# Kernel optimization log

Measured on AMD Instinct MI355X. Metric: run time of the kernel, lower is better.

Reference implementation:

```python
import jax, jax.numpy as jnp
import numpy as np

B, S, HID = 1, 4096, 2048
NH, NKV, D = 16, 4, 128
BLK, M, K_TOP = 64, 32, 8
THETA = 10000.0
NEG = jnp.float32(-1e9)


def setup_inputs() -> dict:
    key = jax.random.key(0)
    ks = jax.random.split(key, 6)
    s = 0.02
    return {
        "hidden_states": jax.random.normal(ks[0], (B, S, HID), jnp.float32),
        "position_ids": jnp.arange(S, dtype=jnp.int32)[None, :],
        "Wq": jax.random.normal(ks[1], (HID, NH * D), jnp.float32) * s,
        "Wk": jax.random.normal(ks[2], (HID, NKV * D), jnp.float32) * s,
        "Wv": jax.random.normal(ks[3], (HID, NKV * D), jnp.float32) * s,
        "Wo": jax.random.normal(ks[4], (NH * D, HID), jnp.float32) * s,
        # seeded random-sign (Hadamard-style) sketch projection, non-trainable buffer
        "H_sketch": jnp.sign(jax.random.normal(ks[5], (D, M), jnp.float32)) / jnp.sqrt(jnp.float32(M)),
    }


def _rot_half(x):
    x1, x2 = x[..., : D // 2], x[..., D // 2 :]
    return jnp.concatenate([-x2, x1], axis=-1)


def reference(hidden_states, position_ids, Wq, Wk, Wv, Wo, H_sketch):
    # QKV projections -> [B, heads, S, D]
    q = (hidden_states @ Wq).reshape(B, S, NH, D).transpose(0, 2, 1, 3)
    k = (hidden_states @ Wk).reshape(B, S, NKV, D).transpose(0, 2, 1, 3)
    v = (hidden_states @ Wv).reshape(B, S, NKV, D).transpose(0, 2, 1, 3)

    # RoPE
    inv_freq = 1.0 / (THETA ** (jnp.arange(0, D, 2, dtype=jnp.float32) / D))
    freqs = position_ids.astype(jnp.float32)[:, :, None] * inv_freq[None, None, :]
    emb = jnp.concatenate([freqs, freqs], axis=-1)  # [B, S, D]
    cos, sin = jnp.cos(emb)[:, None], jnp.sin(emb)[:, None]  # [B, 1, S, D]
    q = q * cos + _rot_half(q) * sin
    k = k * cos + _rot_half(k) * sin

    # GQA repeat kv heads
    rep = NH // NKV
    k = jnp.repeat(k, rep, axis=1)
    v = jnp.repeat(v, rep, axis=1)

    nblk = S // BLK
    # Hadamard-sketch projections, block-mean pooled -> [B, NH, nblk, M]
    Sq = jnp.einsum("bhsd,dm->bhsm", q, H_sketch).reshape(B, NH, nblk, BLK, M).mean(axis=3)
    Sk = jnp.einsum("bhsd,dm->bhsm", k, H_sketch).reshape(B, NH, nblk, BLK, M).mean(axis=3)

    # Block-level sketch scores, causal at block granularity, diagonal forced in
    bs = jnp.einsum("bhim,bhjm->bhij", Sq, Sk)
    blk_causal = jnp.tril(jnp.ones((nblk, nblk), dtype=bool))
    bs = jnp.where(blk_causal, bs, NEG)
    bs = jnp.where(jnp.eye(nblk, dtype=bool), jnp.float32(1e9), bs)
    _, idx = jax.lax.top_k(bs, K_TOP)  # [B, NH, nblk, K_TOP]

    # Gather selected K/V blocks -> [B, NH, nblk, K_TOP, BLK, D]
    K5 = k.reshape(B, NH, nblk, BLK, D)
    V5 = v.reshape(B, NH, nblk, BLK, D)
    gidx = idx[..., None, None]
    Kg = jnp.take_along_axis(K5[:, :, None], gidx, axis=3)
    Vg = jnp.take_along_axis(V5[:, :, None], gidx, axis=3)

    # Block-sparse scores [B, NH, nblk, BLK, K_TOP, BLK]
    Qb = q.reshape(B, NH, nblk, BLK, D)
    scores = jnp.einsum("bhnqd,bhnkcd->bhnqkc", Qb, Kg) / jnp.sqrt(jnp.float32(D))

    # Token-level causal mask over gathered keys
    qpos = jnp.arange(nblk)[:, None] * BLK + jnp.arange(BLK)[None, :]  # [nblk, BLK]
    kpos = idx[..., None] * BLK + jnp.arange(BLK)  # [B, NH, nblk, K_TOP, BLK]
    mask = kpos[:, :, :, None] <= qpos[None, None, :, :, None, None]
    scores = jnp.where(mask, scores, NEG)

    probs = jax.nn.softmax(scores.reshape(B, NH, nblk, BLK, K_TOP * BLK), axis=-1)
    probs = probs.reshape(scores.shape)

    out = jnp.einsum("bhnqkc,bhnkcd->bhnqd", probs, Vg)
    out = out.reshape(B, NH, S, D).transpose(0, 2, 1, 3).reshape(B, S, NH * D)
    return out @ Wo
```

## Files before the change

### kernel.cpp

```cpp
#include <hip/hip_runtime.h>
#include <hip/hip_bf16.h>

#define S_LEN 4096
#define HID 2048
#define NH 16
#define NKV 4
#define HD 128
#define MSK 32
#define KTOP 8
#define NBLK 64
#define NEGV -1000000000.0f
#define SENT -3.0e38f

typedef __hip_bfloat16 bf16;
typedef __attribute__((ext_vector_type(8))) short short8;
typedef __attribute__((ext_vector_type(4))) float f32x4;


__device__ __forceinline__ unsigned short f2b(float v) {
    __hip_bfloat16 h = __float2bfloat16(v);
    return *reinterpret_cast<unsigned short*>(&h);
}
__device__ __forceinline__ float b2f(unsigned short u) {
    return __bfloat162float(*reinterpret_cast<__hip_bfloat16*>(&u));
}
__device__ __forceinline__ void gl16(const void* g, void* l) {
    __builtin_amdgcn_global_load_lds(
        (const __attribute__((address_space(1))) void*)g,
        (__attribute__((address_space(3))) void*)l, 16, 0, 0);
}

__global__ __launch_bounds__(256) void splitW_tiles(
    const float* __restrict__ Wq, const float* __restrict__ Wk,
    const float* __restrict__ Wv,
    bf16* __restrict__ WtqH, bf16* __restrict__ WtqL,
    bf16* __restrict__ WtkH, bf16* __restrict__ WtkL,
    bf16* __restrict__ WtvH) {
    const int u = blockIdx.x, kt = blockIdx.y, k0 = kt * 32;
    const float* W; char* TH; char* TL; int Nd, n0; bool hasLo;
    if (u < 16)      { W = Wq; TH = (char*)WtqH + (size_t)u * 524288;        TL = (char*)WtqL + (size_t)u * 524288; Nd = 2048; n0 = u * 128; hasLo = true; }
    else if (u < 20) { W = Wk; TH = (char*)WtkH + (size_t)(u - 16) * 524288; TL = (char*)WtkL + (size_t)(u - 16) * 524288; Nd = 512; n0 = (u - 16) * 128; hasLo = true; }
    else             { W = Wv; TH = (char*)WtvH + (size_t)(u - 20) * 524288; TL = nullptr; Nd = 512; n0 = (u - 20) * 128; hasLo = false; }
    __shared__ float Lw[32][132];
    const int t = threadIdx.x;
#pragma unroll
    for (int i = 0; i < 4; i++) {
        const int task = t + i * 256;
        const int k = task >> 5, c4 = task & 31;
        *(float4*)&Lw[k][c4 * 4] = *(const float4*)&W[(size_t)(k0 + k) * Nd + n0 + c4 * 4];
    }
    __syncthreads();
#pragma unroll
    for (int i = 0; i < 2; i++) {
        const int task = t + i * 256;
        const int col = task >> 2, lq = task & 3;
        alignas(16) unsigned short hh[8], lo[8];
#pragma unroll
        for (int j = 0; j < 8; j++) {
            const float x = Lw[lq * 8 + j][col];
            hh[j] = f2b(x);
            lo[j] = f2b(x - b2f(hh[j]));
        }
        const size_t off = (size_t)kt * 8192 + (size_t)(((col * 4 + lq) ^ (col & 7))) * 16;
        *(uint4*)(TH + off) = *(const uint4*)hh;
        if (hasLo) *(uint4*)(TL + off) = *(const uint4*)lo;
    }
}

__global__ __launch_bounds__(256) void splitT_Wo(const float* __restrict__ Wo,
                                                 bf16* __restrict__ WtoH) {
    const int n0 = blockIdx.x * 64, k0 = blockIdx.y * 64;
    __shared__ float Ls[64][68];
    const int t = threadIdx.x;
    {
        const int kk = t >> 2, c0 = (t & 3) * 16;
#pragma unroll
        for (int i = 0; i < 4; i++)
            *(float4*)&Ls[kk][c0 + i * 4] =
                *(const float4*)&Wo[(size_t)(k0 + kk) * HID + n0 + c0 + i * 4];
    }
    __syncthreads();
    const int c = t >> 2, ks = (t & 3) * 16;
    alignas(16) unsigned short hh[16];
#pragma unroll
    for (int j = 0; j < 16; j++) hh[j] = f2b(Ls[ks + j][c]);
    unsigned short* TH = (unsigned short*)WtoH;
    const size_t db = (size_t)(n0 + c) * HID + k0 + ks;
    *(uint4*)&TH[db + 0] = *(const uint4*)&hh[0];
    *(uint4*)&TH[db + 8] = *(const uint4*)&hh[8];
}

__global__ __launch_bounds__(256) void splitA_tiles(const float* __restrict__ A,
                                                    bf16* __restrict__ AhiT,
                                                    bf16* __restrict__ AloT) {
    const int rb = blockIdx.x, kt = blockIdx.y;
    const int t = threadIdx.x;
    char* DH = (char*)AhiT + ((size_t)rb * 64 + kt) * 8192;
    char* DL = (char*)AloT + ((size_t)rb * 64 + kt) * 8192;
#pragma unroll
    for (int i = 0; i < 2; i++) {
        const int task = t + i * 256;
        const int row = task >> 2, lq = task & 3;
        const float* ap = &A[(size_t)(rb * 128 + row) * HID + kt * 32 + lq * 8];
        const float4 v0 = *(const float4*)ap;
        const float4 v1 = *(const float4*)(ap + 4);
        const float f[8] = {v0.x, v0.y, v0.z, v0.w, v1.x, v1.y, v1.z, v1.w};
        alignas(16) unsigned short hh[8], lo[8];
#pragma unroll
        for (int j = 0; j < 8; j++) {
            hh[j] = f2b(f[j]);
            lo[j] = f2b(f[j] - b2f(hh[j]));
        }
        const size_t off = (size_t)(((row * 4 + lq) ^ (row & 7))) * 16;
        *(uint4*)(DH + off) = *(const uint4*)hh;
        *(uint4*)(DL + off) = *(const uint4*)lo;
    }
}

__global__ __launch_bounds__(256, 3) void proj4(
    const float* __restrict__ A,
    const bf16* __restrict__ AhiT_, const bf16* __restrict__ AloT_,
    const bf16* __restrict__ WtqH_, const bf16* __restrict__ WtqL_,
    const bf16* __restrict__ WtkH_, const bf16* __restrict__ WtkL_,
    const bf16* __restrict__ WtvH_,
    const int* __restrict__ pos_ids, const float* __restrict__ H,
    bf16* __restrict__ qf, bf16* __restrict__ kf, bf16* __restrict__ vfT,
    float* __restrict__ Sq, float* __restrict__ Sk) {
    const int u = blockIdx.x;
    const bool isQ = (u < 16);
    const bool isV = (u >= 20);
    const bool np3 = !isV;
    const int h = isQ ? u : (isV ? (u - 20) : (u - 16));
    const char* WHb = (const char*)(isQ ? WtqH_ : (isV ? WtvH_ : WtkH_)) + (size_t)h * 524288;
    const char* WLb = (const char*)(isQ ? WtqL_ : WtkL_) + (size_t)h * 524288;
    const char* AHb = (const char*)AhiT_;
    const char* ALb = (const char*)AloT_;
    bf16* __restrict__ Xout = isQ ? qf : kf;
    float* __restrict__ Sout = isQ ? Sq : Sk;
    const int Nd = isQ ? (NH * HD) : (NKV * HD);

    const int rb = blockIdx.y;
    const int m0g = rb * 128;
    const int t = threadIdx.x;
    const int w = t >> 6, L = t & 63;
    const int lm = L & 15, lq = L >> 4;

    __shared__ __align__(16) char arena[34816];
    __shared__ float red[4][128];
    char* Wh_s = arena;
    char* Wl_s = arena + 8192;
    char* Ah_s = arena + 16384;
    char* Al_s = arena + 24576;

    f32x4 acc[2][8];
#pragma unroll
    for (int mt = 0; mt < 2; mt++)
#pragma unroll
        for (int nt = 0; nt < 8; nt++) acc[mt][nt] = (f32x4){0.f, 0.f, 0.f, 0.f};

    for (int kt = 0; kt < 64; kt++) {
        __syncthreads();
        const size_t tW = (size_t)kt * 8192;
#pragma unroll
        for (int i = 0; i < 2; i++) {
            const int so = (w * 2 + i) * 1024;
            gl16(WHb + tW + so + L * 16, Wh_s + so);
            if (np3) gl16(WLb + tW + so + L * 16, Wl_s + so);
        }
        if (AHb) {
            const size_t tA = ((size_t)rb * 64 + kt) * 8192;
#pragma unroll
            for (int i = 0; i < 2; i++) {
                const int so = (w * 2 + i) * 1024;
                gl16(AHb + tA + so + L * 16, Ah_s + so);
                if (np3) gl16(ALb + tA + so + L * 16, Al_s + so);
            }
        } else {
            const int k0 = kt * 32;
#pragma unroll
            for (int i = 0; i < 2; i++) {
                const int task = t + i * 256;
                const int row = task >> 2, q2 = task & 3;
                const float* ap = &A[(size_t)(m0g + row) * HID + k0 + q2 * 8];
                const float4 v0 = *(const float4*)ap;
                const float4 v1 = *(const float4*)(ap + 4);
                const float f[8] = {v0.x, v0.y, v0.z, v0.w, v1.x, v1.y, v1.z, v1.w};
                alignas(16) unsigned short hh[8], lo[8];
#pragma unroll
                for (int j = 0; j < 8; j++) {
                    hh[j] = f2b(f[j]);
                    if (np3) lo[j] = f2b(f[j] - b2f(hh[j]));
                }
                const int ch = ((row * 4 + q2) ^ (row & 7)) * 16;
                *(uint4*)(Ah_s + ch) = *(const uint4*)hh;
                if (np3) *(uint4*)(Al_s + ch) = *(const uint4*)lo;
            }
        }
        __syncthreads();
        const int xr = lm & 7;
        short8 ah[2], al[2];
#pragma unroll
        for (int mt = 0; mt < 2; mt++) {
            const int rowA = w * 32 + mt * 16 + lm;
            const int cA = (((rowA * 4 + lq) ^ xr)) * 16;
            ah[mt] = *(const short8*)(Ah_s + cA);
            if (np3) al[mt] = *(const short8*)(Al_s + cA);
        }
#pragma unroll
        for (int nt = 0; nt < 8; nt++) {
            const int rowW = nt * 16 + lm;
            const int cW = (((rowW * 4 + lq) ^ xr)) * 16;
            const short8 bh = *(const short8*)(Wh_s + cW);
#pragma unroll
            for (int mt = 0; mt < 2; mt++)
                acc[mt][nt] = __builtin_amdgcn_mfma_f32_16x16x32_bf16(ah[mt], bh, acc[mt][nt], 0, 0, 0);
            if (np3) {
                const short8 bl = *(const short8*)(Wl_s + cW);
#pragma unroll
                for (int mt = 0; mt < 2; mt++) {
                    acc[mt][nt] = __builtin_amdgcn_mfma_f32_16x16x32_bf16(ah[mt], bl, acc[mt][nt], 0, 0, 0);
                    acc[mt][nt] = __builtin_amdgcn_mfma_f32_16x16x32_bf16(al[mt], bh, acc[mt][nt], 0, 0, 0);
                }
            }
        }
    }

    if (isV) {
        __syncthreads();
        unsigned short(*Tv)[136] = (unsigned short(*)[136])arena;
#pragma unroll
        for (int mt = 0; mt < 2; mt++) {
            const int rbs = w * 32 + mt * 16 + lq * 4;
#pragma unroll
            for (int rr = 0; rr < 4; rr++)
#pragma unroll
                for (int nt = 0; nt < 8; nt++)
                    Tv[nt * 16 + lm][rbs + rr] = f2b(acc[mt][nt][rr]);
        }
        __syncthreads();
        const int col = t >> 1, rh = (t & 1) * 64;
        bf16* dst = &vfT[((size_t)h * HD + col) * S_LEN + m0g + rh];
#pragma unroll
        for (int u2 = 0; u2 < 8; u2++)
            *(uint4*)&dst[u2 * 8] = *(const uint4*)&Tv[col][rh + u2 * 8];
        return;
    }

    {
        float invf[4];
#pragma unroll
        for (int c4 = 0; c4 < 4; c4++) {
            const int jj = c4 * 16 + lm;
            invf[c4] = 1.0f / powf(10000.0f, (float)jj * (1.0f / 64.0f));
        }
#pragma unroll
        for (int mt = 0; mt < 2; mt++) {
            const int rbase = w * 32 + mt * 16 + lq * 4;
#pragma unroll
            for (int rr = 0; rr < 4; rr++) {
                const float p = (float)pos_ids[m0g + rbase + rr];
#pragma unroll
                for (int c4 = 0; c4 < 4; c4++) {
                    const float fr = p * invf[c4];
                    float sv, cv;
                    sincosf(fr, &sv, &cv);
                    const float x1 = acc[mt][c4][rr];
                    const float x2 = acc[mt][c4 + 4][rr];
                    acc[mt][c4][rr]     = x1 * cv - x2 * sv;
                    acc[mt][c4 + 4][rr] = x2 * cv + x1 * sv;
                }
            }
        }
    }

    float cs[8];
#pragma unroll
    for (int nt = 0; nt < 8; nt++) cs[nt] = 0.f;
#pragma unroll
    for (int mt = 0; mt < 2; mt++) {
        const int rbase = w * 32 + mt * 16 + lq * 4;
#pragma unroll
        for (int rr = 0; rr < 4; rr++) {
            bf16* dst = &Xout[(size_t)(m0g + rbase + rr) * Nd + h * HD + lm];
#pragma unroll
            for (int nt = 0; nt < 8; nt++) {
                const float v = acc[mt][nt][rr];
                dst[nt * 16] = __float2bfloat16(v);
                cs[nt] += v;
            }
        }
    }
#pragma unroll
    for (int nt = 0; nt < 8; nt++) {
        cs[nt] += __shfl_xor(cs[nt], 16);
        cs[nt] += __shfl_xor(cs[nt], 32);
    }
    if (lq == 0) {
#pragma unroll
        for (int nt = 0; nt < 8; nt++) red[w][nt * 16 + lm] = cs[nt];
    }
    __syncthreads();
    if (t < 64) {
        const int b = t >> 5, m = t & 31;
        float s = 0.f;
        for (int d = 0; d < 128; d++)
            s += (red[b * 2][d] + red[b * 2 + 1][d]) * H[d * MSK + m];
        Sout[((size_t)h * NBLK + (m0g >> 6) + b) * MSK + m] = s * (1.0f / 64.0f);
    }
}

__global__ __launch_bounds__(256, 3) void proj_rope_sketch(
    const float* __restrict__ A, const float* __restrict__ Wq,
    const float* __restrict__ Wk, const float* __restrict__ Wv,
    const int* __restrict__ pos_ids, const float* __restrict__ H,
    bf16* __restrict__ qf, bf16* __restrict__ kf, bf16* __restrict__ vf,
    float* __restrict__ Sq, float* __restrict__ Sk,
    int u0, int r0, int xbase) {
    const int u = blockIdx.x + u0;
    const bool isQ = (u < 16);
    const bool isV = (u >= 20);
    const bool np3 = !isV;
    const int h = isQ ? u : (isV ? (u - 20) : (u - 16));
    const float* __restrict__ W = isQ ? Wq : (isV ? Wv : Wk);
    const int Nd = isQ ? (NH * HD) : (NKV * HD);
    bf16* __restrict__ Xout = isQ ? qf : kf;
    float* __restrict__ Sout = isQ ? Sq : Sk;

    const int m0g = r0 + blockIdx.y * 128;
    const int m0x = isQ ? (m0g - xbase) : m0g;
    const int t = threadIdx.x;
    const int w = t >> 6, L = t & 63;
    const int lm = L & 15, lq = L >> 4;

    __shared__ __align__(16) unsigned short shmem[4 * 128 * 40];
    __shared__ float red[4][128];
    unsigned short(*pAh)[40] = (unsigned short(*)[40])(shmem);
    unsigned short(*pAl)[40] = (unsigned short(*)[40])(shmem + 128 * 40);
    unsigned short(*pWh)[40] = (unsigned short(*)[40])(shmem + 2 * 128 * 40);
    unsigned short(*pWl)[40] = (unsigned short(*)[40])(shmem + 3 * 128 * 40);

    f32x4 acc[2][8];
#pragma unroll
    for (int mt = 0; mt < 2; mt++)
#pragma unroll
        for (int nt = 0; nt < 8; nt++) acc[mt][nt] = (f32x4){0.f, 0.f, 0.f, 0.f};

    for (int k0 = 0; k0 < HID; k0 += 32) {
        __syncthreads();
#pragma unroll
        for (int i = 0; i < 4; i++) {
            const int idx = t + i * 256;
            const int row = idx >> 3, f4 = idx & 7;
            const float4 v = *(const float4*)&A[(size_t)(m0g + row) * HID + k0 + f4 * 4];
            ushort4 uh;
            uh.x = f2b(v.x); uh.y = f2b(v.y); uh.z = f2b(v.z); uh.w = f2b(v.w);
            *(ushort4*)&pAh[row][f4 * 4] = uh;
            if (np3) {
                ushort4 ul;
                ul.x = f2b(v.x - b2f(uh.x)); ul.y = f2b(v.y - b2f(uh.y));
                ul.z = f2b(v.z - b2f(uh.z)); ul.w = f2b(v.w - b2f(uh.w));
                *(ushort4*)&pAl[row][f4 * 4] = ul;
            }
        }
        {
            const int wcol = t >> 1, wk0 = (t & 1) * 16;
            const float* wp = &W[(size_t)(k0 + wk0) * Nd + h * HD + wcol];
            alignas(16) unsigned short hh[16];
            alignas(16) unsigned short ll[16];
#pragma unroll
            for (int uu = 0; uu < 16; uu++) {
                const float x = wp[(size_t)uu * Nd];
                hh[uu] = f2b(x);
                ll[uu] = f2b(x - b2f(hh[uu]));
            }
            *(uint4*)&pWh[wcol][wk0 + 0] = *(const uint4*)&hh[0];
            *(uint4*)&pWh[wcol][wk0 + 8] = *(const uint4*)&hh[8];
            if (np3) {
                *(uint4*)&pWl[wcol][wk0 + 0] = *(const uint4*)&ll[0];
                *(uint4*)&pWl[wcol][wk0 + 8] = *(const uint4*)&ll[8];
            }
        }
        __syncthreads();
        short8 ah[2], al[2];
#pragma unroll
        for (int mt = 0; mt < 2; mt++) {
            ah[mt] = *(const short8*)&pAh[w * 32 + mt * 16 + lm][lq * 8];
            if (np3) al[mt] = *(const short8*)&pAl[w * 32 + mt * 16 + lm][lq * 8];
        }
#pragma unroll
        for (int nt = 0; nt < 8; nt++) {
            const short8 bh = *(const short8*)&pWh[nt * 16 + lm][lq * 8];
#pragma unroll
            for (int mt = 0; mt < 2; mt++)
                acc[mt][nt] = __builtin_amdgcn_mfma_f32_16x16x32_bf16(ah[mt], bh, acc[mt][nt], 0, 0, 0);
            if (np3) {
                const short8 bl = *(const short8*)&pWl[nt * 16 + lm][lq * 8];
#pragma unroll
                for (int mt = 0; mt < 2; mt++) {
                    acc[mt][nt] = __builtin_amdgcn_mfma_f32_16x16x32_bf16(ah[mt], bl, acc[mt][nt], 0, 0, 0);
                    acc[mt][nt] = __builtin_amdgcn_mfma_f32_16x16x32_bf16(al[mt], bh, acc[mt][nt], 0, 0, 0);
                }
            }
        }
    }

    if (isV) {
        __syncthreads();
        unsigned short(*Tv)[136] = (unsigned short(*)[136])shmem;
#pragma unroll
        for (int mt = 0; mt < 2; mt++) {
            const int rbs = w * 32 + mt * 16 + lq * 4;
#pragma unroll
            for (int rr = 0; rr < 4; rr++)
#pragma unroll
                for (int nt = 0; nt < 8; nt++)
                    Tv[nt * 16 + lm][rbs + rr] = f2b(acc[mt][nt][rr]);
        }
        __syncthreads();
        const int col = t >> 1, rh = (t & 1) * 64;
        bf16* dst = &vf[((size_t)h * HD + col) * S_LEN + m0g + rh];
#pragma unroll
        for (int u2 = 0; u2 < 8; u2++)
            *(uint4*)&dst[u2 * 8] = *(const uint4*)&Tv[col][rh + u2 * 8];
        return;
    }

    {
        float invf[4];
#pragma unroll
        for (int c4 = 0; c4 < 4; c4++) {
            const int jj = c4 * 16 + lm;
            invf[c4] = 1.0f / powf(10000.0f, (float)jj * (1.0f / 64.0f));
        }
#pragma unroll
        for (int mt = 0; mt < 2; mt++) {
            const int rbase = w * 32 + mt * 16 + lq * 4;
#pragma unroll
            for (int rr = 0; rr < 4; rr++) {
                const float p = (float)pos_ids[m0g + rbase + rr];
#pragma unroll
                for (int c4 = 0; c4 < 4; c4++) {
                    const float fr = p * invf[c4];
                    float sv, cv;
                    sincosf(fr, &sv, &cv);
                    const float x1 = acc[mt][c4][rr];
                    const float x2 = acc[mt][c4 + 4][rr];
                    acc[mt][c4][rr]     = x1 * cv - x2 * sv;
                    acc[mt][c4 + 4][rr] = x2 * cv + x1 * sv;
                }
            }
        }
    }

    float cs[8];
#pragma unroll
    for (int nt = 0; nt < 8; nt++) cs[nt] = 0.f;
#pragma unroll
    for (int mt = 0; mt < 2; mt++) {
        const int rbase = w * 32 + mt * 16 + lq * 4;
#pragma unroll
        for (int rr = 0; rr < 4; rr++) {
            bf16* dst = &Xout[(size_t)(m0x + rbase + rr) * Nd + h * HD + lm];
#pragma unroll
            for (int nt = 0; nt < 8; nt++) {
                const float v = acc[mt][nt][rr];
                dst[nt * 16] = __float2bfloat16(v);
                cs[nt] += v;
            }
        }
    }
#pragma unroll
    for (int nt = 0; nt < 8; nt++) {
        cs[nt] += __shfl_xor(cs[nt], 16);
        cs[nt] += __shfl_xor(cs[nt], 32);
    }
    if (lq == 0) {
#pragma unroll
        for (int nt = 0; nt < 8; nt++) red[w][nt * 16 + lm] = cs[nt];
    }
    __syncthreads();
    if (t < 64) {
        const int b = t >> 5, m = t & 31;
        float s = 0.f;
        for (int d = 0; d < 128; d++)
            s += (red[b * 2][d] + red[b * 2 + 1][d]) * H[d * MSK + m];
        Sout[((size_t)h * NBLK + (m0g >> 6) + b) * MSK + m] = s * (1.0f / 64.0f);
    }
}

__global__ __launch_bounds__(64) void topk_kernel(const float* __restrict__ Sq,
                                                  const float* __restrict__ Sk,
                                                  int* __restrict__ topk, int i0) {
    const int i = i0 + blockIdx.x, h = blockIdx.y, kv = h >> 2;
    const int j = threadIdx.x;
    __shared__ float vals[64];
    float v;
    if (j > i) v = NEGV;
    else if (j == i) v = 1e9f;
    else {
        v = 0.f;
        const float* sq = Sq + ((size_t)h * NBLK + i) * MSK;
        const float* sk = Sk + ((size_t)kv * NBLK + j) * MSK;
        for (int m = 0; m < MSK; m++) v += sq[m] * sk[m];
    }
    vals[j] = v;
    __syncthreads();
    if (j == 0) {
        for (int kk = 0; kk < KTOP; kk++) {
            float best = SENT; int bi = 0;
            for (int jj = 0; jj < 64; jj++)
                if (vals[jj] > best) { best = vals[jj]; bi = jj; }
            vals[bi] = SENT;
            topk[((size_t)h * NBLK + i) * KTOP + kk] = bi;
        }
    }
}

__global__ __launch_bounds__(256) void attn_kernel(bf16* __restrict__ qf,
                                                   const bf16* __restrict__ kf,
                                                   const bf16* __restrict__ vfT,
                                                   const int* __restrict__ topk,
                                                   int r0, int qbase) {
    const int qbg = (r0 >> 6) + blockIdx.x;
    const int h = blockIdx.y, kvh = h >> 2;
    const int t = threadIdx.x;
    const int w = t >> 6, L = t & 63;
    const int lm = L & 15, lq = L >> 4;

    __shared__ __align__(16) unsigned short Ks[64][136];
    __shared__ __align__(16) unsigned short Vt[128][72];
    __shared__ __align__(16) unsigned short Ps[64][72];

    short8 qfrag[4];
    {
        const size_t qrow = (size_t)(qbg * 64 - qbase) + w * 16 + lm;
        const unsigned short* qp = (const unsigned short*)qf + qrow * (NH * HD) + h * HD;
#pragma unroll
        for (int ks = 0; ks < 4; ks++)
            qfrag[ks] = *(const short8*)&qp[ks * 32 + lq * 8];
    }
    f32x4 O[8];
#pragma unroll
    for (int nt = 0; nt < 8; nt++) O[nt] = (f32x4){0.f, 0.f, 0.f, 0.f};
    f32x4 mrow = (f32x4){-1e30f, -1e30f, -1e30f, -1e30f};
    f32x4 lrow = (f32x4){0.f, 0.f, 0.f, 0.f};

    const int* sel = topk + ((size_t)h * NBLK + qbg) * KTOP;
    const int qpos0 = qbg * 64 + w * 16 + lq * 4;
    const float scale = 0.08838834764831845f;

    for (int kb = 0; kb < KTOP; kb++) {
        const int blk = sel[kb] & 63;
        __syncthreads();
#pragma unroll
        for (int i = 0; i < 4; i++) {
            const int idx = t + i * 256;
            const int rr = idx >> 4, c8 = idx & 15;
            *(uint4*)&Ks[rr][c8 * 8] =
                *(const uint4*)&kf[(size_t)(blk * 64 + rr) * (NKV * HD) + kvh * HD + c8 * 8];
        }
#pragma unroll
        for (int i = 0; i < 4; i++) {
            const int idx = t + i * 256;
            const int dd = idx >> 3, j8 = idx & 7;
            *(uint4*)&Vt[dd][j8 * 8] =
                *(const uint4*)&vfT[((size_t)kvh * HD + dd) * S_LEN + blk * 64 + j8 * 8];
        }
        __syncthreads();
        f32x4 S4[4];
#pragma unroll
        for (int nt = 0; nt < 4; nt++) {
            S4[nt] = (f32x4){0.f, 0.f, 0.f, 0.f};
#pragma unroll
            for (int ks = 0; ks < 4; ks++) {
                const short8 bk = *(const short8*)&Ks[nt * 16 + lm][ks * 32 + lq * 8];
                S4[nt] = __builtin_amdgcn_mfma_f32_16x16x32_bf16(qfrag[ks], bk, S4[nt], 0, 0, 0);
            }
        }
#pragma unroll
        for (int nt = 0; nt < 4; nt++) {
            const int kpos = blk * 64 + nt * 16 + lm;
#pragma unroll
            for (int r = 0; r < 4; r++)
                S4[nt][r] = (kpos <= qpos0 + r) ? S4[nt][r] * scale : NEGV;
        }
        f32x4 mx = S4[0];
#pragma unroll
        for (int nt = 1; nt < 4; nt++)
#pragma unroll
            for (int r = 0; r < 4; r++) mx[r] = fmaxf(mx[r], S4[nt][r]);
#pragma unroll
        for (int d = 1; d < 16; d <<= 1)
#pragma unroll
            for (int r = 0; r < 4; r++) mx[r] = fmaxf(mx[r], __shfl_xor(mx[r], d));
        f32x4 mnew, alv, sum;
#pragma unroll
        for (int r = 0; r < 4; r++) {
            mnew[r] = fmaxf(mrow[r], mx[r]);
            alv[r] = __expf(mrow[r] - mnew[r]);
            sum[r] = 0.f;
        }
#pragma unroll
        for (int nt = 0; nt < 4; nt++)
#pragma unroll
            for (int r = 0; r < 4; r++) {
                const float p = __expf(S4[nt][r] - mnew[r]);
                S4[nt][r] = p;
                sum[r] += p;
            }
#pragma unroll
        for (int d = 1; d < 16; d <<= 1)
#pragma unroll
            for (int r = 0; r < 4; r++) sum[r] += __shfl_xor(sum[r], d);
#pragma unroll
        for (int r = 0; r < 4; r++) {
            lrow[r] = lrow[r] * alv[r] + sum[r];
            mrow[r] = mnew[r];
        }
#pragma unroll
        for (int nt = 0; nt < 4; nt++)
#pragma unroll
            for (int r = 0; r < 4; r++)
                Ps[w * 16 + lq * 4 + r][nt * 16 + lm] = f2b(S4[nt][r]);
#pragma unroll
        for (int nt = 0; nt < 8; nt++)
#pragma unroll
            for (int r = 0; r < 4; r++) O[nt][r] *= alv[r];
#pragma unroll
        for (int ks2 = 0; ks2 < 2; ks2++) {
            const short8 pa = *(const short8*)&Ps[w * 16 + lm][ks2 * 32 + lq * 8];
#pragma unroll
            for (int nt = 0; nt < 8; nt++) {
                const short8 vv = *(const short8*)&Vt[nt * 16 + lm][ks2 * 32 + lq * 8];
                O[nt] = __builtin_amdgcn_mfma_f32_16x16x32_bf16(pa, vv, O[nt], 0, 0, 0);
            }
        }
    }
    f32x4 inv;
#pragma unroll
    for (int r = 0; r < 4; r++) inv[r] = 1.0f / lrow[r];
    const size_t orow0 = (size_t)(qbg * 64 - qbase) + w * 16 + lq * 4;
#pragma unroll
    for (int nt = 0; nt < 8; nt++)
#pragma unroll
        for (int r = 0; r < 4; r++)
            qf[(orow0 + r) * (NH * HD) + h * HD + nt * 16 + lm] =
                __float2bfloat16(O[nt][r] * inv[r]);
}

__global__ __launch_bounds__(256) void gemm_out(const bf16* __restrict__ A,
                                                const float* __restrict__ W,
                                                float* __restrict__ C, int cRow0) {
    __shared__ __align__(16) unsigned short Wl[128][40];
    const int n0 = blockIdx.x * 128, m0 = blockIdx.y * 128;
    const int t = threadIdx.x;
    const int w = t >> 6, L = t & 63;
    const int lm = L & 15, lq = L >> 4;
    const int wcol = t >> 1, wk0 = (t & 1) * 16;
    f32x4 acc[2][8];
#pragma unroll
    for (int mt = 0; mt < 2; mt++)
#pragma unroll
        for (int nt = 0; nt < 8; nt++) acc[mt][nt] = (f32x4){0.f, 0.f, 0.f, 0.f};

    float wreg[16];
    {
        const float* wp = &W[(size_t)wk0 * HID + n0 + wcol];
#pragma unroll
        for (int u = 0; u < 16; u++) wreg[u] = wp[(size_t)u * HID];
    }
    short8 av[2];
#pragma unroll
    for (int mt = 0; mt < 2; mt++)
        av[mt] = *(const short8*)&A[(size_t)(m0 + w * 32 + mt * 16 + lm) * HID + lq * 8];

    for (int k0 = 0; k0 < HID; k0 += 32) {
        __syncthreads();
        {
            alignas(16) unsigned short hh[16];
#pragma unroll
            for (int u = 0; u < 16; u++) hh[u] = f2b(wreg[u]);
            *(uint4*)&Wl[wcol][wk0 + 0] = *(const uint4*)&hh[0];
            *(uint4*)&Wl[wcol][wk0 + 8] = *(const uint4*)&hh[8];
        }
        const int k1 = k0 + 32;
        if (k1 < HID) {
            const float* wp = &W[(size_t)(k1 + wk0) * HID + n0 + wcol];
#pragma unroll
            for (int u = 0; u < 16; u++) wreg[u] = wp[(size_t)u * HID];
        }
        __syncthreads();
        short8 avn[2];
        if (k1 < HID) {
#pragma unroll
            for (int mt = 0; mt < 2; mt++)
                avn[mt] = *(const short8*)&A[(size_t)(m0 + w * 32 + mt * 16 + lm) * HID + k1 + lq * 8];
        }
#pragma unroll
        for (int nt = 0; nt < 8; nt++) {
            const short8 bv = *(const short8*)&Wl[nt * 16 + lm][lq * 8];
#pragma unroll
            for (int mt = 0; mt < 2; mt++)
                acc[mt][nt] = __builtin_amdgcn_mfma_f32_16x16x32_bf16(av[mt], bv, acc[mt][nt], 0, 0, 0);
        }
        if (k1 < HID) { av[0] = avn[0]; av[1] = avn[1]; }
    }
#pragma unroll
    for (int mt = 0; mt < 2; mt++)
#pragma unroll
        for (int nt = 0; nt < 8; nt++)
#pragma unroll
            for (int r = 0; r < 4; r++) {
                const int row = m0 + w * 32 + mt * 16 + lq * 4 + r;
                C[(size_t)(cRow0 + row) * HID + n0 + nt * 16 + lm] = acc[mt][nt][r];
            }
}

__global__ __launch_bounds__(256) void gemm_out2(const bf16* __restrict__ A,
                                                 const bf16* __restrict__ WtoH,
                                                 float* __restrict__ C) {
    __shared__ __align__(16) unsigned short Wl[128][72];
    const int n0 = blockIdx.x * 128, m0 = blockIdx.y * 128;
    const int t = threadIdx.x;
    const int w = t >> 6, L = t & 63;
    const int lm = L & 15, lq = L >> 4;
    const int ct = t >> 1, sg = (t & 1) * 32;
    const unsigned short* __restrict__ WT = (const unsigned short*)WtoH;
    f32x4 acc[2][8];
#pragma unroll
    for (int mt = 0; mt < 2; mt++)
#pragma unroll
        for (int nt = 0; nt < 8; nt++) acc[mt][nt] = (f32x4){0.f, 0.f, 0.f, 0.f};

    uint4 wbuf[4];
    {
        const unsigned short* wp = &WT[(size_t)(n0 + ct) * HID + sg];
#pragma unroll
        for (int i = 0; i < 4; i++) wbuf[i] = *(const uint4*)&wp[i * 8];
    }
    short8 av[2][2];
#pragma unroll
    for (int mt = 0; mt < 2; mt++)
#pragma unroll
        for (int ks = 0; ks < 2; ks++)
            av[mt][ks] = *(const short8*)&A[(size_t)(m0 + w * 32 + mt * 16 + lm) * HID + ks * 32 + lq * 8];

    for (int k0 = 0; k0 < HID; k0 += 64) {
        __syncthreads();
#pragma unroll
        for (int i = 0; i < 4; i++) *(uint4*)&Wl[ct][sg + i * 8] = wbuf[i];
        const int k1 = k0 + 64;
        if (k1 < HID) {
            const unsigned short* wp = &WT[(size_t)(n0 + ct) * HID + k1 + sg];
#pragma unroll
            for (int i = 0; i < 4; i++) wbuf[i] = *(const uint4*)&wp[i * 8];
        }
        __syncthreads();
        short8 avn[2][2];
        if (k1 < HID) {
#pragma unroll
            for (int mt = 0; mt < 2; mt++)
#pragma unroll
                for (int ks = 0; ks < 2; ks++)
                    avn[mt][ks] = *(const short8*)&A[(size_t)(m0 + w * 32 + mt * 16 + lm) * HID + k1 + ks * 32 + lq * 8];
        }
#pragma unroll
        for (int ks = 0; ks < 2; ks++)
#pragma unroll
            for (int nt = 0; nt < 8; nt++) {
                const short8 bv = *(const short8*)&Wl[nt * 16 + lm][ks * 32 + lq * 8];
#pragma unroll
                for (int mt = 0; mt < 2; mt++)
                    acc[mt][nt] = __builtin_amdgcn_mfma_f32_16x16x32_bf16(av[mt][ks], bv, acc[mt][nt], 0, 0, 0);
            }
        if (k1 < HID) {
#pragma unroll
            for (int mt = 0; mt < 2; mt++)
#pragma unroll
                for (int ks = 0; ks < 2; ks++) av[mt][ks] = avn[mt][ks];
        }
    }
#pragma unroll
    for (int mt = 0; mt < 2; mt++)
#pragma unroll
        for (int nt = 0; nt < 8; nt++)
#pragma unroll
            for (int r = 0; r < 4; r++) {
                const int row = m0 + w * 32 + mt * 16 + lq * 4 + r;
                C[(size_t)row * HID + n0 + nt * 16 + lm] = acc[mt][nt][r];
            }
}

extern "C" void kernel_launch(void* const* d_in, const int* in_sizes, int n_in,
                              void* d_out, int out_size, void* d_ws, size_t ws_size,
                              hipStream_t stream) {
    const void *p_hid, *p_pos, *p_wq, *p_wk, *p_wv, *p_wo, *p_h;
    if (in_sizes[0] == 4096 && in_sizes[1] == 1048576) {
        p_h = d_in[0]; p_wk = d_in[1]; p_wo = d_in[2]; p_wq = d_in[3];
        p_wv = d_in[4]; p_hid = d_in[5]; p_pos = d_in[6];
    } else {
        p_hid = d_in[0]; p_pos = d_in[1]; p_wq = d_in[2]; p_wk = d_in[3];
        p_wv = d_in[4]; p_wo = d_in[5]; p_h = d_in[6];
    }
    const float* hidden = (const float*)p_hid;
    const int* pos_ids  = (const int*)p_pos;
    const float* Wq = (const float*)p_wq;
    const float* Wk = (const float*)p_wk;
    const float* Wv = (const float*)p_wv;
    const float* Wo = (const float*)p_wo;
    const float* Hsk = (const float*)p_h;
    float* out = (float*)d_out;

    char* base = (char*)d_ws;
    float* Sq    = (float*)base;
    float* Sk    = (float*)(base + 131072);
    int*   topkb = (int*)(base + 163840);
    bf16*  kf    = (bf16*)(base + 196608);
    bf16*  vfT   = (bf16*)(base + 196608 + 4194304);
    bf16*  qbuf  = (bf16*)(base + 196608 + 8388608);
    bf16*  WtqH  = (bf16*)(base + 25362432);
    bf16*  WtqL  = (bf16*)(base + 33751040);
    bf16*  WtkH  = (bf16*)(base + 42139648);
    bf16*  WtkL  = (bf16*)(base + 44236800);
    bf16*  WtvH  = (bf16*)(base + 46333952);
    bf16*  WtoH  = (bf16*)(base + 48431104);
    bf16*  AhiT  = (bf16*)(base + 56819712);
    bf16*  AloT  = (bf16*)(base + 73596928);
    const size_t FULL_NEED  = 25362432;
    const size_t FULL2_NEED = 48431104;
    const size_t FULL3_NEED = 56819712;
    const size_t FULL4_NEED = 90374144;

    if (ws_size >= FULL2_NEED) {
        const bool hasWo = (ws_size >= FULL3_NEED);
        const bool hasA  = (ws_size >= FULL4_NEED);
        splitW_tiles<<<dim3(24, 64), 256, 0, stream>>>(
            Wq, Wk, Wv, WtqH, WtqL, WtkH, WtkL, WtvH);
        if (hasWo)
            splitT_Wo<<<dim3(32, 32), 256, 0, stream>>>(Wo, WtoH);
        if (hasA)
            splitA_tiles<<<dim3(32, 64), 256, 0, stream>>>(hidden, AhiT, AloT);
        proj4<<<dim3(24, 32), 256, 0, stream>>>(
            hidden, hasA ? AhiT : nullptr, hasA ? AloT : nullptr,
            WtqH, WtqL, WtkH, WtkL, WtvH, pos_ids, Hsk,
            qbuf, kf, vfT, Sq, Sk);
        topk_kernel<<<dim3(NBLK, NH), 64, 0, stream>>>(Sq, Sk, topkb, 0);
        attn_kernel<<<dim3(NBLK, NH), 256, 0, stream>>>(
            qbuf, kf, vfT, topkb, 0, 0);
        if (hasWo)
            gemm_out2<<<dim3(HID / 128, S_LEN / 128), 256, 0, stream>>>(
                qbuf, WtoH, out);
        else
            gemm_out<<<dim3(HID / 128, S_LEN / 128), 256, 0, stream>>>(
                qbuf, Wo, out, 0);
    } else if (ws_size >= FULL_NEED) {
        proj_rope_sketch<<<dim3(24, S_LEN / 128), 256, 0, stream>>>(
            hidden, Wq, Wk, Wv, pos_ids, Hsk, qbuf, kf, vfT, Sq, Sk, 0, 0, 0);
        topk_kernel<<<dim3(NBLK, NH), 64, 0, stream>>>(Sq, Sk, topkb, 0);
        attn_kernel<<<dim3(NBLK, NH), 256, 0, stream>>>(
            qbuf, kf, vfT, topkb, 0, 0);
        gemm_out<<<dim3(HID / 128, S_LEN / 128), 256, 0, stream>>>(
            qbuf, Wo, out, 0);
    } else {
        proj_rope_sketch<<<dim3(8, S_LEN / 128), 256, 0, stream>>>(
            hidden, Wq, Wk, Wv, pos_ids, Hsk, qbuf, kf, vfT, Sq, Sk, 16, 0, 0);
        for (int c = 0; c < 16; c++) {
            const int r0 = c * 256;
            proj_rope_sketch<<<dim3(16, 2), 256, 0, stream>>>(
                hidden, Wq, Wk, Wv, pos_ids, Hsk, qbuf, kf, vfT, Sq, Sk, 0, r0, r0);
            topk_kernel<<<dim3(4, NH), 64, 0, stream>>>(Sq, Sk, topkb, r0 >> 6);
            attn_kernel<<<dim3(4, NH), 256, 0, stream>>>(
                qbuf, kf, vfT, topkb, r0, r0);
            gemm_out<<<dim3(HID / 128, 2), 256, 0, stream>>>(
                qbuf, Wo, out, r0);
        }
    }
}
```

Measured before the change: 460.9 us.

## Swizzle block ids for XCD locality, prefetch K/V in attention, shrink output GEMM tile

The projection, attention and output GEMM kernels now use a 1-D grid, and each kernel remaps its block id with an XCD-style swizzle. The intent is for blocks that share weights or KV heads to run on the same chiplet and hit the same L2. The attention kernel register-prefetches the next selected K/V block while computing on the current one, and raises wave priority around the MFMA sections. The output GEMM tile narrows from 128 to 64 columns, doubling the block count to 1024 for better occupancy, at the cost of less reuse of A per block.

```diff
diff --git a/kernel.cpp b/kernel.cpp
--- a/kernel.cpp
+++ b/kernel.cpp
@@ -126,7 +126,10 @@
     const int* __restrict__ pos_ids, const float* __restrict__ H,
     bf16* __restrict__ qf, bf16* __restrict__ kf, bf16* __restrict__ vfT,
     float* __restrict__ Sq, float* __restrict__ Sk) {
-    const int u = blockIdx.x;
+    const int id = blockIdx.x;
+    const int swz = (id & 7) * 96 + (id >> 3);
+    const int u = swz >> 5;
+    const int rb = swz & 31;
     const bool isQ = (u < 16);
     const bool isV = (u >= 20);
     const bool np3 = !isV;
@@ -139,7 +142,6 @@
     float* __restrict__ Sout = isQ ? Sq : Sk;
     const int Nd = isQ ? (NH * HD) : (NKV * HD);
 
-    const int rb = blockIdx.y;
     const int m0g = rb * 128;
     const int t = threadIdx.x;
     const int w = t >> 6, L = t & 63;
@@ -521,8 +523,17 @@
                                                    const bf16* __restrict__ vfT,
                                                    const int* __restrict__ topk,
                                                    int r0, int qbase) {
-    const int qbg = (r0 >> 6) + blockIdx.x;
-    const int h = blockIdx.y, kvh = h >> 2;
+    int qbg, h;
+    if (gridDim.y == 1) {
+        const int id = blockIdx.x;
+        const int swz = (id & 7) * 128 + (id >> 3);
+        h = swz >> 6;
+        qbg = swz & 63;
+    } else {
+        qbg = (r0 >> 6) + blockIdx.x;
+        h = blockIdx.y;
+    }
+    const int kvh = h >> 2;
     const int t = threadIdx.x;
     const int w = t >> 6, L = t & 63;
     const int lm = L & 15, lq = L >> 4;
@@ -549,25 +560,38 @@
     const int qpos0 = qbg * 64 + w * 16 + lq * 4;
     const float scale = 0.08838834764831845f;
 
+    const int rrK0 = t >> 4, c8K = t & 15;
+    const int ddV0 = t >> 3, j8V = t & 7;
+    uint4 kreg[4], vreg[4];
+    int blk = sel[0] & 63;
+    {
+#pragma unroll
+        for (int i = 0; i < 4; i++)
+            kreg[i] = *(const uint4*)&kf[(size_t)(blk * 64 + rrK0 + i * 16) * (NKV * HD) + kvh * HD + c8K * 8];
+#pragma unroll
+        for (int i = 0; i < 4; i++)
+            vreg[i] = *(const uint4*)&vfT[((size_t)kvh * HD + ddV0 + i * 32) * S_LEN + blk * 64 + j8V * 8];
+    }
+
     for (int kb = 0; kb < KTOP; kb++) {
-        const int blk = sel[kb] & 63;
-        __syncthreads();
-#pragma unroll
-        for (int i = 0; i < 4; i++) {
-            const int idx = t + i * 256;
-            const int rr = idx >> 4, c8 = idx & 15;
-            *(uint4*)&Ks[rr][c8 * 8] =
-                *(const uint4*)&kf[(size_t)(blk * 64 + rr) * (NKV * HD) + kvh * HD + c8 * 8];
-        }
-#pragma unroll
-        for (int i = 0; i < 4; i++) {
-            const int idx = t + i * 256;
-            const int dd = idx >> 3, j8 = idx & 7;
-            *(uint4*)&Vt[dd][j8 * 8] =
-                *(const uint4*)&vfT[((size_t)kvh * HD + dd) * S_LEN + blk * 64 + j8 * 8];
-        }
-        __syncthreads();
+        const int cur_blk = blk;
+        __syncthreads();
+#pragma unroll
+        for (int i = 0; i < 4; i++) *(uint4*)&Ks[rrK0 + i * 16][c8K * 8] = kreg[i];
+#pragma unroll
+        for (int i = 0; i < 4; i++) *(uint4*)&Vt[ddV0 + i * 32][j8V * 8] = vreg[i];
+        __syncthreads();
+        if (kb + 1 < KTOP) {
+            blk = sel[kb + 1] & 63;
+#pragma unroll
+            for (int i = 0; i < 4; i++)
+                kreg[i] = *(const uint4*)&kf[(size_t)(blk * 64 + rrK0 + i * 16) * (NKV * HD) + kvh * HD + c8K * 8];
+#pragma unroll
+            for (int i = 0; i < 4; i++)
+                vreg[i] = *(const uint4*)&vfT[((size_t)kvh * HD + ddV0 + i * 32) * S_LEN + blk * 64 + j8V * 8];
+        }
         f32x4 S4[4];
+        __builtin_amdgcn_s_setprio(1);
 #pragma unroll
         for (int nt = 0; nt < 4; nt++) {
             S4[nt] = (f32x4){0.f, 0.f, 0.f, 0.f};
@@ -577,9 +601,10 @@
                 S4[nt] = __builtin_amdgcn_mfma_f32_16x16x32_bf16(qfrag[ks], bk, S4[nt], 0, 0, 0);
             }
         }
+        __builtin_amdgcn_s_setprio(0);
 #pragma unroll
         for (int nt = 0; nt < 4; nt++) {
-            const int kpos = blk * 64 + nt * 16 + lm;
+            const int kpos = cur_blk * 64 + nt * 16 + lm;
 #pragma unroll
             for (int r = 0; r < 4; r++)
                 S4[nt][r] = (kpos <= qpos0 + r) ? S4[nt][r] * scale : NEGV;
@@ -626,6 +651,7 @@
         for (int nt = 0; nt < 8; nt++)
 #pragma unroll
             for (int r = 0; r < 4; r++) O[nt][r] *= alv[r];
+        __builtin_amdgcn_s_setprio(1);
 #pragma unroll
         for (int ks2 = 0; ks2 < 2; ks2++) {
             const short8 pa = *(const short8*)&Ps[w * 16 + lm][ks2 * 32 + lq * 8];
@@ -635,6 +661,7 @@
                 O[nt] = __builtin_amdgcn_mfma_f32_16x16x32_bf16(pa, vv, O[nt], 0, 0, 0);
             }
         }
+        __builtin_amdgcn_s_setprio(0);
     }
     f32x4 inv;
 #pragma unroll
@@ -719,24 +746,27 @@
 __global__ __launch_bounds__(256) void gemm_out2(const bf16* __restrict__ A,
                                                  const bf16* __restrict__ WtoH,
                                                  float* __restrict__ C) {
-    __shared__ __align__(16) unsigned short Wl[128][72];
-    const int n0 = blockIdx.x * 128, m0 = blockIdx.y * 128;
+    const int id = blockIdx.x;
+    const int swz = (id & 7) * 128 + (id >> 3);
+    const int rb = swz >> 5, np = swz & 31;
+    const int n0 = np * 64, m0 = rb * 128;
+    __shared__ __align__(16) unsigned short Wl[64][72];
     const int t = threadIdx.x;
     const int w = t >> 6, L = t & 63;
     const int lm = L & 15, lq = L >> 4;
-    const int ct = t >> 1, sg = (t & 1) * 32;
+    const int ct = t >> 2, sg = (t & 3) * 16;
     const unsigned short* __restrict__ WT = (const unsigned short*)WtoH;
-    f32x4 acc[2][8];
+    f32x4 acc[2][4];
 #pragma unroll
     for (int mt = 0; mt < 2; mt++)
 #pragma unroll
-        for (int nt = 0; nt < 8; nt++) acc[mt][nt] = (f32x4){0.f, 0.f, 0.f, 0.f};
-
-    uint4 wbuf[4];
+        for (int nt = 0; nt < 4; nt++) acc[mt][nt] = (f32x4){0.f, 0.f, 0.f, 0.f};
+
+    uint4 wbuf[2];
     {
         const unsigned short* wp = &WT[(size_t)(n0 + ct) * HID + sg];
-#pragma unroll
-        for (int i = 0; i < 4; i++) wbuf[i] = *(const uint4*)&wp[i * 8];
+        wbuf[0] = *(const uint4*)&wp[0];
+        wbuf[1] = *(const uint4*)&wp[8];
     }
     short8 av[2][2];
 #pragma unroll
@@ -747,13 +777,13 @@
 
     for (int k0 = 0; k0 < HID; k0 += 64) {
         __syncthreads();
-#pragma unroll
-        for (int i = 0; i < 4; i++) *(uint4*)&Wl[ct][sg + i * 8] = wbuf[i];
+        *(uint4*)&Wl[ct][sg + 0] = wbuf[0];
+        *(uint4*)&Wl[ct][sg + 8] = wbuf[1];
         const int k1 = k0 + 64;
         if (k1 < HID) {
             const unsigned short* wp = &WT[(size_t)(n0 + ct) * HID + k1 + sg];
-#pragma unroll
-            for (int i = 0; i < 4; i++) wbuf[i] = *(const uint4*)&wp[i * 8];
+            wbuf[0] = *(const uint4*)&wp[0];
+            wbuf[1] = *(const uint4*)&wp[8];
         }
         __syncthreads();
         short8 avn[2][2];
@@ -767,7 +797,7 @@
 #pragma unroll
         for (int ks = 0; ks < 2; ks++)
 #pragma unroll
-            for (int nt = 0; nt < 8; nt++) {
+            for (int nt = 0; nt < 4; nt++) {
                 const short8 bv = *(const short8*)&Wl[nt * 16 + lm][ks * 32 + lq * 8];
 #pragma unroll
                 for (int mt = 0; mt < 2; mt++)
@@ -783,7 +813,7 @@
 #pragma unroll
     for (int mt = 0; mt < 2; mt++)
 #pragma unroll
-        for (int nt = 0; nt < 8; nt++)
+        for (int nt = 0; nt < 4; nt++)
 #pragma unroll
             for (int r = 0; r < 4; r++) {
                 const int row = m0 + w * 32 + mt * 16 + lq * 4 + r;
@@ -840,16 +870,15 @@
             splitT_Wo<<<dim3(32, 32), 256, 0, stream>>>(Wo, WtoH);
         if (hasA)
             splitA_tiles<<<dim3(32, 64), 256, 0, stream>>>(hidden, AhiT, AloT);
-        proj4<<<dim3(24, 32), 256, 0, stream>>>(
+        proj4<<<dim3(768), 256, 0, stream>>>(
             hidden, hasA ? AhiT : nullptr, hasA ? AloT : nullptr,
             WtqH, WtqL, WtkH, WtkL, WtvH, pos_ids, Hsk,
             qbuf, kf, vfT, Sq, Sk);
         topk_kernel<<<dim3(NBLK, NH), 64, 0, stream>>>(Sq, Sk, topkb, 0);
-        attn_kernel<<<dim3(NBLK, NH), 256, 0, stream>>>(
+        attn_kernel<<<dim3(1024), 256, 0, stream>>>(
             qbuf, kf, vfT, topkb, 0, 0);
         if (hasWo)
-            gemm_out2<<<dim3(HID / 128, S_LEN / 128), 256, 0, stream>>>(
-                qbuf, WtoH, out);
+            gemm_out2<<<dim3(1024), 256, 0, stream>>>(qbuf, WtoH, out);
         else
             gemm_out<<<dim3(HID / 128, S_LEN / 128), 256, 0, stream>>>(
                 qbuf, Wo, out, 0);
```

Result: slower. 475.1 us (+3.1%).
